# Kernel tuning notes

Hardware: AMD Instinct MI355X
Metric: run time of the kernel (lower is better)

Reference implementation:

```python
import jax, jax.numpy as jnp
import numpy as np

DIM = 512
HEADS = 8
DHEAD = DIM // HEADS
M = DIM // 2          # num_landmarks = 256
ITERS = 6             # pinv iterations
KSIZE = 33            # residual conv kernel (seq axis)
EPS = 1e-5            # LayerNorm eps (torch default)


def moore_penrose_pinv(a, iters=ITERS):
    # a: [b, h, m, m]; iterative Newton-Schulz style pseudo-inverse
    abs_a = jnp.abs(a)
    col = abs_a.sum(-1).max()   # global max of row-sums
    row = abs_a.sum(-2).max()   # global max of col-sums
    z = jnp.swapaxes(a, -1, -2) / (col * row)
    I = jnp.eye(a.shape[-1], dtype=a.dtype)

    def body(z, _):
        az = a @ z
        z = 0.25 * z @ (13.0 * I - az @ (15.0 * I - az @ (7.0 * I - az)))
        return z, None

    z, _ = jax.lax.scan(body, z, None, length=iters)
    return z


def res_conv(v, conv_w):
    # v: [b, h, n, d] treated as NCHW (C=heads), depthwise kernel (33, 1)
    return jax.lax.conv_general_dilated(
        v, conv_w, window_strides=(1, 1),
        padding=((KSIZE // 2, KSIZE // 2), (0, 0)),
        dimension_numbers=('NCHW', 'OIHW', 'NCHW'),
        feature_group_count=HEADS)


def setup_inputs() -> dict:
    key = jax.random.key(0)
    ks = jax.random.split(key, 5)
    b, n = 4, 4096  # n % M == 0 -> no padding branch
    x = jax.random.normal(ks[0], (b, n, DIM), jnp.float32)
    norm_w = jnp.ones((DIM,), jnp.float32)
    norm_b = jnp.zeros((DIM,), jnp.float32)
    Wqkv = jax.random.normal(ks[1], (DIM, 3 * DIM), jnp.float32) * (DIM ** -0.5)
    Wout = jax.random.normal(ks[2], (DIM, DIM), jnp.float32) * (DIM ** -0.5)
    bout = jnp.zeros((DIM,), jnp.float32)
    conv_w = jax.random.normal(ks[3], (HEADS, 1, KSIZE, 1), jnp.float32) * 0.05
    return {"x": x, "norm_w": norm_w, "norm_b": norm_b,
            "Wqkv": Wqkv, "Wout": Wout, "bout": bout, "conv_w": conv_w}


def reference(x, norm_w, norm_b, Wqkv, Wout, bout, conv_w):
    b, n, dim = x.shape
    # LayerNorm
    mu = x.mean(-1, keepdims=True)
    var = ((x - mu) ** 2).mean(-1, keepdims=True)
    xn = (x - mu) * jax.lax.rsqrt(var + EPS) * norm_w + norm_b

    # QKV projection, split heads: [b, h, n, d]
    qkv = xn @ Wqkv
    q, k, v = jnp.split(qkv, 3, axis=-1)
    sh = lambda t: t.reshape(b, n, HEADS, DHEAD).transpose(0, 2, 1, 3)
    q, k, v = sh(q), sh(k), sh(v)
    q = q * (DHEAD ** -0.5)

    # landmarks: mean over consecutive segments of length l = n // M
    l = n // M
    q_l = q.reshape(b, HEADS, M, l, DHEAD).mean(3)  # [b,h,m,d]
    k_l = k.reshape(b, HEADS, M, l, DHEAD).mean(3)

    sim1 = jnp.einsum('bhid,bhjd->bhij', q, k_l)    # [b,h,n,m]
    sim2 = jnp.einsum('bhid,bhjd->bhij', q_l, k_l)  # [b,h,m,m]
    sim3 = jnp.einsum('bhid,bhjd->bhij', q_l, k)    # [b,h,m,n]
    a1 = jax.nn.softmax(sim1, axis=-1)
    a2 = jax.nn.softmax(sim2, axis=-1)
    a3 = jax.nn.softmax(sim3, axis=-1)

    a2_inv = moore_penrose_pinv(a2)
    out = (a1 @ a2_inv) @ (a3 @ v)                  # [b,h,n,d]
    out = out + res_conv(v, conv_w)                  # residual depthwise conv on v

    out = out.transpose(0, 2, 1, 3).reshape(b, n, dim)
    out = out @ Wout + bout                          # to_out (dropout = identity in eval)
    return x + out                                   # TransLayer residual
```

## Files before the change

### kernel.cpp

```cpp
#include <hip/hip_runtime.h>
#include <hip/hip_bf16.h>

#define BB 4
#define NN 4096
#define DIMM 512
#define HH 8
#define DD 64
#define MM 256
#define LL 16
#define BHH 32
#define NROW (BB*NN)
#define KS 33

typedef __attribute__((ext_vector_type(8))) short short8;
typedef __attribute__((ext_vector_type(4))) float float4v;

static __device__ __forceinline__ unsigned short bf16_bits(float v) {
    __hip_bfloat16 h = __float2bfloat16(v);
    return *reinterpret_cast<unsigned short*>(&h);
}

static __device__ __forceinline__ void unpack_bf2(unsigned w, float& lo, float& hi) {
    lo = __uint_as_float(w << 16);
    hi = __uint_as_float(w & 0xffff0000u);
}

static __device__ __forceinline__ void gl_lds16(const void* g, void* l) {
    __builtin_amdgcn_global_load_lds((const __attribute__((address_space(1))) void*)g,
                                     (__attribute__((address_space(3))) void*)l, 16, 0, 0);
}

__launch_bounds__(256)
__global__ void ln_kernel(const float* __restrict__ x,
                          const float* __restrict__ w,
                          const float* __restrict__ bvec,
                          __hip_bfloat16* __restrict__ xn) {
    int row = blockIdx.x;
    int t = threadIdx.x;
    const float* xr = x + (long)row * DIMM;
    float v0 = xr[t];
    float v1 = xr[t + 256];
    __shared__ float red[256];
    red[t] = v0 + v1;
    __syncthreads();
    for (int off = 128; off > 0; off >>= 1) { if (t < off) red[t] += red[t + off]; __syncthreads(); }
    float mu = red[0] * (1.0f / DIMM);
    __syncthreads();
    float d0 = v0 - mu, d1 = v1 - mu;
    red[t] = d0 * d0 + d1 * d1;
    __syncthreads();
    for (int off = 128; off > 0; off >>= 1) { if (t < off) red[t] += red[t + off]; __syncthreads(); }
    float var = red[0] * (1.0f / DIMM);
    float rs = rsqrtf(var + 1e-5f);
    xn[(long)row * DIMM + t]       = __float2bfloat16(d0 * rs * w[t]       + bvec[t]);
    xn[(long)row * DIMM + t + 256] = __float2bfloat16(d1 * rs * w[t + 256] + bvec[t + 256]);
}

__launch_bounds__(256)
__global__ void transpose_bf16(const float* __restrict__ in, __hip_bfloat16* __restrict__ outp,
                               int K, int N) {
    __shared__ float tile[32][33];
    int k0 = blockIdx.y * 32, n0 = blockIdx.x * 32;
    int tx = threadIdx.x & 31, ty = threadIdx.x >> 5;
    #pragma unroll
    for (int i = 0; i < 32; i += 8)
        tile[ty + i][tx] = in[(long)(k0 + ty + i) * N + n0 + tx];
    __syncthreads();
    #pragma unroll
    for (int i = 0; i < 32; i += 8)
        outp[(long)(n0 + ty + i) * K + k0 + tx] = __float2bfloat16(tile[tx][ty + i]);
}

enum { EPI_NONE = 0, EPI_QKV = 1, EPI_OUT = 2 };

template<int EPI>
__launch_bounds__(256)
__global__ void gemm_mfma(const __hip_bfloat16* __restrict__ A,
                          const __hip_bfloat16* __restrict__ Bt,
                          float* __restrict__ C, int M, int N, int K,
                          const float* __restrict__ bias,
                          const float* __restrict__ resid,
                          __hip_bfloat16* __restrict__ qb,
                          __hip_bfloat16* __restrict__ kb,
                          __hip_bfloat16* __restrict__ vtb) {
    __shared__ __hip_bfloat16 As[128][64];
    __shared__ __hip_bfloat16 Bs[128][64];
    const int t = threadIdx.x;
    const int m0 = blockIdx.y * 128, n0 = blockIdx.x * 128;
    const int wave = t >> 6, lane = t & 63;
    const int wrow = wave >> 1, wcol = wave & 1;
    const int lm = lane & 15, quad = lane >> 4;
    const int wbase = wave * 64;

    float4v acc[4][4] = {};

    for (int k0 = 0; k0 < K; k0 += 64) {
        #pragma unroll
        for (int p = 0; p < 4; ++p) {
            int idx = t + p * 256;
            int r = idx >> 3;
            int csrc = ((idx & 7) ^ (r & 7)) * 8;
            int cb = (p * 256 + wbase) * 8;
            gl_lds16(&A[(long)(m0 + r) * K + k0 + csrc], &As[0][0] + cb);
            gl_lds16(&Bt[(long)(n0 + r) * K + k0 + csrc], &Bs[0][0] + cb);
        }
        __syncthreads();
        #pragma unroll
        for (int ks = 0; ks < 64; ks += 32) {
            short8 af[4], bfr[4];
            #pragma unroll
            for (int i = 0; i < 4; ++i) {
                int ra = wrow * 64 + i * 16 + lm;
                int rb = wcol * 64 + i * 16 + lm;
                int g  = (ks >> 3) + quad;
                af[i]  = *(const short8*)&As[ra][(g ^ (ra & 7)) * 8];
                bfr[i] = *(const short8*)&Bs[rb][(g ^ (rb & 7)) * 8];
            }
            #pragma unroll
            for (int i = 0; i < 4; ++i)
                #pragma unroll
                for (int j = 0; j < 4; ++j)
                    acc[i][j] = __builtin_amdgcn_mfma_f32_16x16x32_bf16(af[i], bfr[j], acc[i][j], 0, 0, 0);
        }
        __syncthreads();
    }

    #pragma unroll
    for (int i = 0; i < 4; ++i) {
        #pragma unroll
        for (int j = 0; j < 4; ++j) {
            int rowb = m0 + wrow * 64 + i * 16 + quad * 4;
            int col  = n0 + wcol * 64 + j * 16 + lm;
            if (EPI == EPI_QKV) {
                int b = rowb >> 12, seq = rowb & (NN - 1);
                int which = col >> 9, rem = col & 511;
                int h = rem >> 6, dd = rem & 63;
                int bh = b * HH + h;
                if (which == 0) {
                    #pragma unroll
                    for (int r = 0; r < 4; ++r)
                        qb[((long)bh * NN + seq + r) * DD + dd] = __float2bfloat16(acc[i][j][r] * 0.125f);
                } else if (which == 1) {
                    #pragma unroll
                    for (int r = 0; r < 4; ++r)
                        kb[((long)bh * NN + seq + r) * DD + dd] = __float2bfloat16(acc[i][j][r]);
                } else {
                    union { unsigned long long u; unsigned short s[4]; } pk;
                    #pragma unroll
                    for (int r = 0; r < 4; ++r) pk.s[r] = bf16_bits(acc[i][j][r]);
                    *(unsigned long long*)&vtb[((long)bh * DD + dd) * NN + seq] = pk.u;
                }
            } else {
                #pragma unroll
                for (int r = 0; r < 4; ++r) {
                    int row = rowb + r;
                    C[(long)row * N + col] = acc[i][j][r] + bias[col] + resid[(long)row * N + col];
                }
            }
        }
    }
}

__launch_bounds__(256)
__global__ void gemm_pinv(const __hip_bfloat16* __restrict__ A,
                          const __hip_bfloat16* __restrict__ Bt,
                          __hip_bfloat16* __restrict__ CnBf,
                          float* __restrict__ CnF,
                          __hip_bfloat16* __restrict__ CTbf,
                          float diag, float sgn, float scale) {
    __shared__ __hip_bfloat16 As[64][256];
    __shared__ __hip_bfloat16 Bs[64][256];
    const int t = threadIdx.x;
    const long base = (long)blockIdx.z << 16;
    const int m0 = blockIdx.y * 64, n0 = blockIdx.x * 64;
    const int wave = t >> 6, lane = t & 63;
    const int wr = wave >> 1, wc = wave & 1;
    const int lm = lane & 15, quad = lane >> 4;
    const __hip_bfloat16* Ab = A + base;
    const __hip_bfloat16* Bb = Bt + base;

    #pragma unroll
    for (int p = 0; p < 8; ++p) {
        int idx = t + p * 256;
        int r = idx >> 5;
        int csrc = ((idx & 31) ^ (r & 7)) * 8;
        int cb = idx * 8;
        gl_lds16(&Ab[(long)(m0 + r) * 256 + csrc], &As[0][0] + cb);
        gl_lds16(&Bb[(long)(n0 + r) * 256 + csrc], &Bs[0][0] + cb);
    }
    __syncthreads();

    float4v acc[2][2] = {};
    #pragma unroll
    for (int ks = 0; ks < 256; ks += 32) {
        short8 af[2], bfr[2];
        #pragma unroll
        for (int i = 0; i < 2; ++i) {
            int ra = wr * 32 + i * 16 + lm;
            int rb = wc * 32 + i * 16 + lm;
            int g  = (ks >> 3) + quad;
            af[i]  = *(const short8*)&As[ra][(g ^ (ra & 7)) * 8];
            bfr[i] = *(const short8*)&Bs[rb][(g ^ (rb & 7)) * 8];
        }
        #pragma unroll
        for (int i = 0; i < 2; ++i)
            #pragma unroll
            for (int j = 0; j < 2; ++j)
                acc[i][j] = __builtin_amdgcn_mfma_f32_16x16x32_bf16(af[i], bfr[j], acc[i][j], 0, 0, 0);
    }

    #pragma unroll
    for (int i = 0; i < 2; ++i)
        #pragma unroll
        for (int j = 0; j < 2; ++j) {
            const int rowb = wr * 32 + i * 16 + quad * 4;
            const int col  = wc * 32 + j * 16 + lm;
            union { unsigned long long u; unsigned short s[4]; } pk;
            #pragma unroll
            for (int r = 0; r < 4; ++r) {
                float v = acc[i][j][r] * scale;
                long off = base + (long)(m0 + rowb + r) * 256 + n0 + col;
                if (CnBf) CnBf[off] = __float2bfloat16(v);
                if (CnF)  CnF[off]  = v;
                float tv = sgn * v + ((m0 + rowb + r) == (n0 + col) ? diag : 0.0f);
                pk.s[r] = bf16_bits(tv);
            }
            if (CTbf)
                *(unsigned long long*)&CTbf[base + (long)(n0 + col) * 256 + m0 + rowb] = pk.u;
        }
}

__launch_bounds__(256)
__global__ void pinv_prep(const float* __restrict__ a2, const float* __restrict__ scl,
                          __hip_bfloat16* __restrict__ a2bf, __hip_bfloat16* __restrict__ z0T,
                          __hip_bfloat16* __restrict__ z0n) {
    __shared__ float tl[64][65];
    const int t = threadIdx.x;
    const long base = (long)blockIdx.z << 16;
    const int i0 = blockIdx.y * 64, j0 = blockIdx.x * 64;
    float s = scl[0];
    #pragma unroll
    for (int p = 0; p < 16; ++p) {
        int idx = t + p * 256;
        int r = idx >> 6, c = idx & 63;
        long off = base + (long)(i0 + r) * 256 + j0 + c;
        float v = a2[off];
        a2bf[off] = __float2bfloat16(v);
        float zv = v * s;
        z0T[off] = __float2bfloat16(zv);
        tl[r][c] = zv;
    }
    __syncthreads();
    int r = t & 63;
    #pragma unroll
    for (int u = 0; u < 16; ++u) {
        int c = u * 4 + (t >> 6);
        z0n[base + (long)(j0 + c) * 256 + i0 + r] = __float2bfloat16(tl[r][c]);
    }
}

template<int EPI, bool TRANSB>
__launch_bounds__(256)
__global__ void gemm64(const float* __restrict__ A, const float* __restrict__ Bm,
                       float* __restrict__ C,
                       int M, int N, int K, long sA, long sB, long sC, float alpha) {
    const int bz = blockIdx.z;
    const float* Ab = A + (long)bz * sA;
    const float* Bb = Bm + (long)bz * sB;
    float* Cb = C + (long)bz * sC;

    __shared__ float As[16][64];
    __shared__ float Bs[16][64];

    const int tid = threadIdx.x;
    const int tx = tid & 15;
    const int ty = tid >> 4;
    const int m0 = blockIdx.y * 64;
    const int n0 = blockIdx.x * 64;

    float acc[4][4] = {};

    for (int k0 = 0; k0 < K; k0 += 16) {
        {
            int r  = tid >> 2;
            int kk = (tid & 3) * 4;
            float4 va = *(const float4*)(Ab + (long)(m0 + r) * K + k0 + kk);
            As[kk + 0][r] = va.x; As[kk + 1][r] = va.y; As[kk + 2][r] = va.z; As[kk + 3][r] = va.w;
        }
        if (!TRANSB) {
            int kk = tid >> 4;
            int j  = (tid & 15) * 4;
            float4 vb = *(const float4*)(Bb + (long)(k0 + kk) * N + n0 + j);
            Bs[kk][j + 0] = vb.x; Bs[kk][j + 1] = vb.y; Bs[kk][j + 2] = vb.z; Bs[kk][j + 3] = vb.w;
        } else {
            int j  = tid >> 2;
            int kk = (tid & 3) * 4;
            float4 vb = *(const float4*)(Bb + (long)(n0 + j) * K + k0 + kk);
            Bs[kk + 0][j] = vb.x; Bs[kk + 1][j] = vb.y; Bs[kk + 2][j] = vb.z; Bs[kk + 3][j] = vb.w;
        }
        __syncthreads();
        #pragma unroll
        for (int kk = 0; kk < 16; ++kk) {
            float a0 = As[kk][ty * 4 + 0], a1 = As[kk][ty * 4 + 1];
            float a2 = As[kk][ty * 4 + 2], a3 = As[kk][ty * 4 + 3];
            float b0 = Bs[kk][tx * 4 + 0], b1 = Bs[kk][tx * 4 + 1];
            float b2 = Bs[kk][tx * 4 + 2], b3 = Bs[kk][tx * 4 + 3];
            acc[0][0] += a0 * b0; acc[0][1] += a0 * b1; acc[0][2] += a0 * b2; acc[0][3] += a0 * b3;
            acc[1][0] += a1 * b0; acc[1][1] += a1 * b1; acc[1][2] += a1 * b2; acc[1][3] += a1 * b3;
            acc[2][0] += a2 * b0; acc[2][1] += a2 * b1; acc[2][2] += a2 * b2; acc[2][3] += a2 * b3;
            acc[3][0] += a3 * b0; acc[3][1] += a3 * b1; acc[3][2] += a3 * b2; acc[3][3] += a3 * b3;
        }
        __syncthreads();
    }

    #pragma unroll
    for (int r = 0; r < 4; ++r)
        #pragma unroll
        for (int c = 0; c < 4; ++c)
            Cb[(long)(m0 + ty * 4 + r) * N + n0 + tx * 4 + c] = acc[r][c] * alpha;
}

__global__ void landmark_kernel(const __hip_bfloat16* __restrict__ qb,
                                const __hip_bfloat16* __restrict__ kb,
                                float* __restrict__ q_l, float* __restrict__ k_l,
                                __hip_bfloat16* __restrict__ q_lb,
                                __hip_bfloat16* __restrict__ k_lb) {
    int bh = blockIdx.x >> 8;
    int m  = blockIdx.x & 255;
    int d  = threadIdx.x;
    const __hip_bfloat16* src = (blockIdx.y ? kb : qb) + ((long)bh * NN + m * LL) * DD + d;
    float s = 0.f;
    #pragma unroll
    for (int t = 0; t < LL; ++t) s += __bfloat162float(src[(long)t * DD]);
    s *= (1.0f / LL);
    long off = ((long)bh * MM + m) * DD + d;
    if (blockIdx.y) { k_l[off] = s; k_lb[off] = __float2bfloat16(s); }
    else            { q_l[off] = s; q_lb[off] = __float2bfloat16(s); }
}

__launch_bounds__(256)
__global__ void softmax256_kernel(float* __restrict__ a) {
    long row = blockIdx.x;
    int t = threadIdx.x;
    float* r = a + row * 256;
    float v = r[t];
    __shared__ float red[256];
    red[t] = v;
    __syncthreads();
    for (int off = 128; off > 0; off >>= 1) { if (t < off) red[t] = fmaxf(red[t], red[t + off]); __syncthreads(); }
    float mx = red[0];
    __syncthreads();
    float e = __expf(v - mx);
    red[t] = e;
    __syncthreads();
    for (int off = 128; off > 0; off >>= 1) { if (t < off) red[t] += red[t + off]; __syncthreads(); }
    r[t] = e / red[0];
}

__launch_bounds__(256)
__global__ void redmax_kernel(const float* __restrict__ a2, float* __restrict__ red) {
    int bh = blockIdx.x;
    int t = threadIdx.x;
    const float* Ab = a2 + ((long)bh << 16);
    float cs = 0.f;
    for (int r = 0; r < 256; ++r) cs += Ab[r * 256 + t];
    __shared__ float m2[256];
    m2[t] = cs;
    __syncthreads();
    for (int off = 128; off > 0; off >>= 1) {
        if (t < off) m2[t] = fmaxf(m2[t], m2[t + off]);
        __syncthreads();
    }
    if (t == 0) red[bh] = m2[0];
}

__global__ void scale_kernel(const float* __restrict__ red, float* __restrict__ scl) {
    __shared__ float b[32];
    int t = threadIdx.x;
    b[t] = red[t];
    __syncthreads();
    for (int off = 16; off > 0; off >>= 1) {
        if (t < off) b[t] = fmaxf(b[t], b[t + off]);
        __syncthreads();
    }
    if (t == 0) scl[0] = 1.0f / b[0];
}

__launch_bounds__(256)
__global__ void a3v_mfma(const __hip_bfloat16* __restrict__ qlb,
                         const __hip_bfloat16* __restrict__ kb,
                         const __hip_bfloat16* __restrict__ vtb,
                         float* __restrict__ opart, float* __restrict__ lpart) {
    const int bh = blockIdx.y;
    const int mt = blockIdx.x >> 2;
    const int ns = blockIdx.x & 3;
    const int t = threadIdx.x;
    const int wave = t >> 6, lane = t & 63;
    const int wr = wave >> 1, wc = wave & 1;
    const int lm = lane & 15, quad = lane >> 4;

    __shared__ __hip_bfloat16 Qs[64][72];
    __shared__ __hip_bfloat16 Ks[64][72];
    __shared__ __hip_bfloat16 Vt[64][72];
    __shared__ __hip_bfloat16 Ps[64][72];
    __shared__ float lred[64][32];

    {
        int r = t >> 3, c8 = (t & 7) * 8;
        const __hip_bfloat16* qbase = qlb + ((long)bh * MM + mt * 64) * DD;
        *(uint4*)&Qs[r][c8]      = *(const uint4*)&qbase[(long)r * DD + c8];
        *(uint4*)&Qs[r + 32][c8] = *(const uint4*)&qbase[(long)(r + 32) * DD + c8];
    }

    float4v acc[2][2] = {};
    float lacc[2][4] = {};
    const __hip_bfloat16* kbase = kb + ((long)bh * NN + ns * 1024) * DD;
    const __hip_bfloat16* vbase = vtb + (long)bh * DD * NN + ns * 1024;
    __syncthreads();

    for (int ch = 0; ch < 16; ++ch) {
        {
            int r = t >> 3, c8 = (t & 7) * 8;
            *(uint4*)&Ks[r][c8]      = *(const uint4*)&kbase[(long)(ch * 64 + r) * DD + c8];
            *(uint4*)&Ks[r + 32][c8] = *(const uint4*)&kbase[(long)(ch * 64 + r + 32) * DD + c8];
            *(uint4*)&Vt[r][c8]      = *(const uint4*)&vbase[(long)r * NN + ch * 64 + c8];
            *(uint4*)&Vt[r + 32][c8] = *(const uint4*)&vbase[(long)(r + 32) * NN + ch * 64 + c8];
        }
        __syncthreads();

        float4v s[2][2] = {};
        #pragma unroll
        for (int ks = 0; ks < 64; ks += 32) {
            short8 af[2], bfr[2];
            #pragma unroll
            for (int i = 0; i < 2; ++i) {
                af[i]  = *(const short8*)&Qs[wr * 32 + i * 16 + lm][ks + quad * 8];
                bfr[i] = *(const short8*)&Ks[wc * 32 + i * 16 + lm][ks + quad * 8];
            }
            #pragma unroll
            for (int i = 0; i < 2; ++i)
                #pragma unroll
                for (int j = 0; j < 2; ++j)
                    s[i][j] = __builtin_amdgcn_mfma_f32_16x16x32_bf16(af[i], bfr[j], s[i][j], 0, 0, 0);
        }
        #pragma unroll
        for (int i = 0; i < 2; ++i)
            #pragma unroll
            for (int j = 0; j < 2; ++j)
                #pragma unroll
                for (int r2 = 0; r2 < 4; ++r2) {
                    float e = __expf(s[i][j][r2]);
                    lacc[i][r2] += e;
                    Ps[wr * 32 + i * 16 + quad * 4 + r2][wc * 32 + j * 16 + lm] = __float2bfloat16(e);
                }
        __syncthreads();

        #pragma unroll
        for (int ks = 0; ks < 64; ks += 32) {
            short8 af[2], bfr[2];
            #pragma unroll
            for (int i = 0; i < 2; ++i) {
                af[i]  = *(const short8*)&Ps[wr * 32 + i * 16 + lm][ks + quad * 8];
                bfr[i] = *(const short8*)&Vt[wc * 32 + i * 16 + lm][ks + quad * 8];
            }
            #pragma unroll
            for (int i = 0; i < 2; ++i)
                #pragma unroll
                for (int j = 0; j < 2; ++j)
                    acc[i][j] = __builtin_amdgcn_mfma_f32_16x16x32_bf16(af[i], bfr[j], acc[i][j], 0, 0, 0);
        }
        __syncthreads();
    }

    #pragma unroll
    for (int i = 0; i < 2; ++i)
        #pragma unroll
        for (int r2 = 0; r2 < 4; ++r2)
            lred[wr * 32 + i * 16 + quad * 4 + r2][wc * 16 + lm] = lacc[i][r2];
    __syncthreads();
    if (t < 64) {
        float s = 0.f;
        #pragma unroll
        for (int u = 0; u < 32; ++u) s += lred[t][u];
        lpart[((bh * 4 + mt) * 4 + ns) * 64 + t] = s;
    }
    const long pbase = ((long)((bh * 4 + mt) * 4 + ns)) << 12;
    #pragma unroll
    for (int i = 0; i < 2; ++i)
        #pragma unroll
        for (int j = 0; j < 2; ++j)
            #pragma unroll
            for (int r2 = 0; r2 < 4; ++r2)
                opart[pbase + (long)(wr * 32 + i * 16 + quad * 4 + r2) * 64 + wc * 32 + j * 16 + lm] = acc[i][j][r2];
}

__global__ void a3v_combine(const float* __restrict__ opart, const float* __restrict__ lpart,
                            float* __restrict__ a3v) {
    int idx = blockIdx.x * 256 + threadIdx.x;
    int d  = idx & 63;
    int m  = (idx >> 6) & 255;
    int bh = idx >> 14;
    int mt = m >> 6, r = m & 63;
    int pb = (bh * 4 + mt) * 4;
    float osum = 0.f, lsum = 0.f;
    #pragma unroll
    for (int ns = 0; ns < 4; ++ns) {
        osum += opart[(((long)(pb + ns)) << 12) + r * 64 + d];
        lsum += lpart[(pb + ns) * 64 + r];
    }
    a3v[((long)bh * MM + m) * DD + d] = osum / lsum;
}

__launch_bounds__(256)
__global__ void wmT_kernel(const float* __restrict__ wm, __hip_bfloat16* __restrict__ wtb) {
    __shared__ float tile[64][65];
    const int bh = blockIdx.x;
    const int t = threadIdx.x;
    for (int mc = 0; mc < 4; ++mc) {
        #pragma unroll
        for (int p = 0; p < 16; ++p) {
            int idx = t + p * 256;
            int r = idx >> 6, c = idx & 63;
            tile[r][c] = wm[((long)bh * MM + mc * 64 + r) * DD + c];
        }
        __syncthreads();
        #pragma unroll
        for (int p = 0; p < 16; ++p) {
            int idx = t + p * 256;
            int dd = idx >> 6, m = idx & 63;
            wtb[((long)bh * DD + dd) * MM + mc * 64 + m] = __float2bfloat16(tile[m][dd]);
        }
        __syncthreads();
    }
}

__launch_bounds__(256)
__global__ void attn_out_mfma(const __hip_bfloat16* __restrict__ qb,
                              const __hip_bfloat16* __restrict__ klb,
                              const __hip_bfloat16* __restrict__ wtb,
                              const __hip_bfloat16* __restrict__ vtb,
                              const float* __restrict__ convw,
                              __hip_bfloat16* __restrict__ ctx) {
    const int bh = blockIdx.y;
    const int b = bh >> 3, h = bh & 7;
    const int i0 = blockIdx.x * 64;
    const int t = threadIdx.x;
    const int wave = t >> 6, lane = t & 63;
    const int wr = wave >> 1, wc = wave & 1;
    const int lm = lane & 15, quad = lane >> 4;

    __shared__ __hip_bfloat16 Qs[64][72];
    __shared__ __hip_bfloat16 Ks[64][72];
    __shared__ __hip_bfloat16 Wt[64][72];
    __shared__ __hip_bfloat16 Ps[64][72];
    __shared__ __hip_bfloat16 Vc[64][104];
    __shared__ float lredS[64][2];
    __shared__ float dsum[64];
    __shared__ float cwS[KS];

    if (t < KS) cwS[t] = convw[h * KS + t];

    {
        int r = t >> 3, c8 = (t & 7) * 8;
        const __hip_bfloat16* qbase = qb + ((long)bh * NN + i0) * DD;
        *(uint4*)&Qs[r][c8]      = *(const uint4*)&qbase[(long)r * DD + c8];
        *(uint4*)&Qs[r + 32][c8] = *(const uint4*)&qbase[(long)(r + 32) * DD + c8];
    }
    {
        for (int c = t; c < 768; c += 256) {
            int dd = c / 12, u = c - dd * 12;
            int g0 = i0 - 16 + u * 8;
            const __hip_bfloat16* vrow = vtb + ((long)bh * DD + dd) * NN;
            __align__(16) __hip_bfloat16 tmp[8];
            if (g0 >= 0 && g0 + 8 <= NN) {
                *(uint4*)tmp = *(const uint4*)&vrow[g0];
            } else {
                #pragma unroll
                for (int e = 0; e < 8; ++e) {
                    int g = g0 + e;
                    tmp[e] = (g >= 0 && g < NN) ? vrow[g] : __float2bfloat16(0.f);
                }
            }
            *(uint4*)&Vc[dd][u * 8] = *(uint4*)tmp;
        }
    }

    float4v acc[2][2] = {};
    float lacc[2][4] = {};
    const __hip_bfloat16* klbase = klb + (long)bh * MM * DD;
    const __hip_bfloat16* wbase  = wtb + (long)bh * DD * MM;
    __syncthreads();

    float cwr[KS];
    #pragma unroll
    for (int k = 0; k < KS; ++k) cwr[k] = cwS[k];

    for (int ch = 0; ch < 4; ++ch) {
        {
            int r = t >> 3, c8 = (t & 7) * 8;
            *(uint4*)&Ks[r][c8]      = *(const uint4*)&klbase[(long)(ch * 64 + r) * DD + c8];
            *(uint4*)&Ks[r + 32][c8] = *(const uint4*)&klbase[(long)(ch * 64 + r + 32) * DD + c8];
            *(uint4*)&Wt[r][c8]      = *(const uint4*)&wbase[(long)r * MM + ch * 64 + c8];
            *(uint4*)&Wt[r + 32][c8] = *(const uint4*)&wbase[(long)(r + 32) * MM + ch * 64 + c8];
        }
        __syncthreads();

        float4v s[2][2] = {};
        #pragma unroll
        for (int ks = 0; ks < 64; ks += 32) {
            short8 af[2], bfr[2];
            #pragma unroll
            for (int i = 0; i < 2; ++i) {
                af[i]  = *(const short8*)&Qs[wr * 32 + i * 16 + lm][ks + quad * 8];
                bfr[i] = *(const short8*)&Ks[wc * 32 + i * 16 + lm][ks + quad * 8];
            }
            #pragma unroll
            for (int i = 0; i < 2; ++i)
                #pragma unroll
                for (int j = 0; j < 2; ++j)
                    s[i][j] = __builtin_amdgcn_mfma_f32_16x16x32_bf16(af[i], bfr[j], s[i][j], 0, 0, 0);
        }
        #pragma unroll
        for (int i = 0; i < 2; ++i)
            #pragma unroll
            for (int j = 0; j < 2; ++j)
                #pragma unroll
                for (int r2 = 0; r2 < 4; ++r2) {
                    float e = __expf(s[i][j][r2]);
                    lacc[i][r2] += e;
                    Ps[wr * 32 + i * 16 + quad * 4 + r2][wc * 32 + j * 16 + lm] = __float2bfloat16(e);
                }
        __syncthreads();

        #pragma unroll
        for (int ks = 0; ks < 64; ks += 32) {
            short8 af[2], bfr[2];
            #pragma unroll
            for (int i = 0; i < 2; ++i) {
                af[i]  = *(const short8*)&Ps[wr * 32 + i * 16 + lm][ks + quad * 8];
                bfr[i] = *(const short8*)&Wt[wc * 32 + i * 16 + lm][ks + quad * 8];
            }
            #pragma unroll
            for (int i = 0; i < 2; ++i)
                #pragma unroll
                for (int j = 0; j < 2; ++j)
                    acc[i][j] = __builtin_amdgcn_mfma_f32_16x16x32_bf16(af[i], bfr[j], acc[i][j], 0, 0, 0);
        }
        __syncthreads();
    }

    #pragma unroll
    for (int i = 0; i < 2; ++i)
        #pragma unroll
        for (int r2 = 0; r2 < 4; ++r2) {
            float s = lacc[i][r2];
            s += __shfl_xor(s, 1);
            s += __shfl_xor(s, 2);
            s += __shfl_xor(s, 4);
            s += __shfl_xor(s, 8);
            if (lm == 0) lredS[wr * 32 + i * 16 + quad * 4 + r2][wc] = s;
        }
    __syncthreads();
    if (t < 64) dsum[t] = 1.0f / (lredS[t][0] + lredS[t][1]);
    __syncthreads();

    #pragma unroll
    for (int j = 0; j < 2; ++j) {
        int dd = wc * 32 + j * 16 + lm;
        #pragma unroll
        for (int i = 0; i < 2; ++i) {
            int R = wr * 32 + i * 16 + quad * 4;
            float X[36];
            #pragma unroll
            for (int u = 0; u < 9; ++u) {
                uint2 wv = *(const uint2*)&Vc[dd][R + u * 4];
                unpack_bf2(wv.x, X[u * 4 + 0], X[u * 4 + 1]);
                unpack_bf2(wv.y, X[u * 4 + 2], X[u * 4 + 3]);
            }
            float co[4] = {};
            #pragma unroll
            for (int k = 0; k < KS; ++k) {
                float c = cwr[k];
                co[0] += c * X[k + 0];
                co[1] += c * X[k + 1];
                co[2] += c * X[k + 2];
                co[3] += c * X[k + 3];
            }
            #pragma unroll
            for (int r2 = 0; r2 < 4; ++r2) {
                int row = R + r2;
                ctx[((long)b * NN + i0 + row) * DIMM + h * DD + dd] =
                    __float2bfloat16(acc[i][j][r2] * dsum[row] + co[r2]);
            }
        }
    }
}

extern "C" void kernel_launch(void* const* d_in, const int* in_sizes, int n_in,
                              void* d_out, int out_size, void* d_ws, size_t ws_size,
                              hipStream_t stream) {
    const float* x      = (const float*)d_in[0];
    const float* norm_w = (const float*)d_in[1];
    const float* norm_b = (const float*)d_in[2];
    const float* Wqkv   = (const float*)d_in[3];
    const float* Wout   = (const float*)d_in[4];
    const float* bout   = (const float*)d_in[5];
    const float* conv_w = (const float*)d_in[6];
    float* out = (float*)d_out;

    float* ws = (float*)d_ws;
    size_t o = 0;
    auto alloc = [&](size_t n) { float* p = ws + o; o += n; return p; };
    auto allocb = [&](size_t n) { return (__hip_bfloat16*)alloc((n + 1) / 2); };

    __hip_bfloat16* xn_bf  = allocb((size_t)NROW * DIMM);
    __hip_bfloat16* wqt_bf = allocb((size_t)3 * DIMM * DIMM);
    __hip_bfloat16* wot_bf = allocb((size_t)DIMM * DIMM);
    __hip_bfloat16* ctx_bf = allocb((size_t)NROW * DIMM);
    __hip_bfloat16* q_bf   = allocb((size_t)BHH * NN * DD);
    __hip_bfloat16* k_bf   = allocb((size_t)BHH * NN * DD);
    __hip_bfloat16* vt_bf  = allocb((size_t)BHH * DD * NN);
    __hip_bfloat16* qlb    = allocb((size_t)BHH * MM * DD);
    __hip_bfloat16* klb    = allocb((size_t)BHH * MM * DD);
    __hip_bfloat16* wt_bf  = allocb((size_t)BHH * DD * MM);
    float* q_l  = alloc((size_t)BHH * MM * DD);
    float* k_l  = alloc((size_t)BHH * MM * DD);
    float* a2   = alloc((size_t)BHH * MM * MM);
    float* zb   = alloc((size_t)BHH * MM * MM);
    float* az   = alloc((size_t)BHH * MM * MM);
    float* gb   = alloc((size_t)BHH * MM * MM);
    float* tb   = alloc((size_t)BHH * MM * MM);
    float* z2   = alloc((size_t)BHH * MM * MM);
    float* a3v  = alloc((size_t)BHH * MM * DD);
    float* wm   = alloc((size_t)BHH * MM * DD);
    float* opart = alloc((size_t)BHH * 4 * 4 * 64 * 64);
    float* lpart = alloc((size_t)BHH * 4 * 4 * 64);
    float* red  = alloc(64);
    float* scl  = alloc(64);

    const size_t HB = 1048576;
    __hip_bfloat16* a2bf = (__hip_bfloat16*)az;
    __hip_bfloat16* znA  = (__hip_bfloat16*)(az + HB);
    __hip_bfloat16* znB  = (__hip_bfloat16*)gb;
    __hip_bfloat16* zTA  = (__hip_bfloat16*)(gb + HB);
    __hip_bfloat16* zTB  = (__hip_bfloat16*)tb;
    __hip_bfloat16* azbf = (__hip_bfloat16*)(tb + HB);
    __hip_bfloat16* g1T  = (__hip_bfloat16*)z2;
    __hip_bfloat16* g2T  = (__hip_bfloat16*)(z2 + HB);
    __hip_bfloat16* g3T  = (__hip_bfloat16*)opart;

    ln_kernel<<<NROW, 256, 0, stream>>>(x, norm_w, norm_b, xn_bf);

    transpose_bf16<<<dim3(3 * DIMM / 32, DIMM / 32), 256, 0, stream>>>(Wqkv, wqt_bf, DIMM, 3 * DIMM);
    transpose_bf16<<<dim3(DIMM / 32, DIMM / 32), 256, 0, stream>>>(Wout, wot_bf, DIMM, DIMM);

    gemm_mfma<EPI_QKV><<<dim3(3 * DIMM / 128, NROW / 128), 256, 0, stream>>>(
        xn_bf, wqt_bf, nullptr, NROW, 3 * DIMM, DIMM,
        nullptr, nullptr, q_bf, k_bf, vt_bf);

    landmark_kernel<<<dim3(BHH * MM, 2), 64, 0, stream>>>(q_bf, k_bf, q_l, k_l, qlb, klb);

    gemm64<EPI_NONE, true><<<dim3(4, 4, BHH), 256, 0, stream>>>(
        q_l, k_l, a2, MM, MM, DD, (long)MM * DD, (long)MM * DD, (long)MM * MM, 1.0f);

    softmax256_kernel<<<BHH * MM, 256, 0, stream>>>(a2);

    redmax_kernel<<<BHH, 256, 0, stream>>>(a2, red);
    scale_kernel<<<1, 32, 0, stream>>>(red, scl);

    dim3 g512(4, 4, BHH);
    pinv_prep<<<g512, 256, 0, stream>>>(a2, scl, a2bf, zTA, znA);

    __hip_bfloat16 *zn = znA, *zT = zTA, *zn2 = znB, *zT2 = zTB;
    for (int it = 0; it < 6; ++it) {
        gemm_pinv<<<g512, 256, 0, stream>>>(a2bf, zT, azbf, nullptr, g1T, 7.0f, -1.0f, 1.0f);
        gemm_pinv<<<g512, 256, 0, stream>>>(azbf, g1T, nullptr, nullptr, g2T, 15.0f, -1.0f, 1.0f);
        gemm_pinv<<<g512, 256, 0, stream>>>(azbf, g2T, nullptr, nullptr, g3T, 13.0f, -1.0f, 1.0f);
        gemm_pinv<<<g512, 256, 0, stream>>>(zn, g3T, zn2, (it == 5) ? zb : nullptr, zT2,
                                            0.0f, 1.0f, 0.25f);
        __hip_bfloat16* tmp;
        tmp = zn; zn = zn2; zn2 = tmp;
        tmp = zT; zT = zT2; zT2 = tmp;
    }

    a3v_mfma<<<dim3(16, BHH), 256, 0, stream>>>(qlb, k_bf, vt_bf, opart, lpart);
    a3v_combine<<<BHH * MM * DD / 256, 256, 0, stream>>>(opart, lpart, a3v);

    gemm64<EPI_NONE, false><<<dim3(1, 4, BHH), 256, 0, stream>>>(
        zb, a3v, wm, MM, DD, MM, (long)MM * MM, (long)MM * DD, (long)MM * DD, 1.0f);
    wmT_kernel<<<BHH, 256, 0, stream>>>(wm, wt_bf);

    attn_out_mfma<<<dim3(NN / 64, BHH), 256, 0, stream>>>(
        q_bf, klb, wt_bf, vt_bf, conv_w, ctx_bf);

    gemm_mfma<EPI_OUT><<<dim3(DIMM / 128, NROW / 128), 256, 0, stream>>>(
        ctx_bf, wot_bf, out, NROW, DIMM, DIMM,
        bout, x, nullptr, nullptr, nullptr);
}
```

Measured before the change: 464.6 us.

## Retile pinv GEMM to 128x128 k-looped tiles and run residual conv on MFMA

The pinv GEMM goes from 64x64 output tiles that load the full K=256 into LDS at once to 128x128 tiles that loop over K in 64-wide chunks. This reduces LDS per block and redundant global reads, but cuts the grid from 512 to 128 blocks per launch. Separately, the 33-tap depthwise residual conv in attn_out is recast as a banded Toeplitz matrix in LDS and computed with bf16 MFMAs instead of scalar FMAs. This removes register pressure and FMA work, at the cost of extra LDS and bf16 rounding of the conv weights.

```diff
diff --git a/kernel.cpp b/kernel.cpp
--- a/kernel.cpp
+++ b/kernel.cpp
@@ -18,11 +18,6 @@
 static __device__ __forceinline__ unsigned short bf16_bits(float v) {
     __hip_bfloat16 h = __float2bfloat16(v);
     return *reinterpret_cast<unsigned short*>(&h);
-}
-
-static __device__ __forceinline__ void unpack_bf2(unsigned w, float& lo, float& hi) {
-    lo = __uint_as_float(w << 16);
-    hi = __uint_as_float(w & 0xffff0000u);
 }
 
 static __device__ __forceinline__ void gl_lds16(const void* g, void* l) {
@@ -168,65 +163,69 @@
                           float* __restrict__ CnF,
                           __hip_bfloat16* __restrict__ CTbf,
                           float diag, float sgn, float scale) {
-    __shared__ __hip_bfloat16 As[64][256];
-    __shared__ __hip_bfloat16 Bs[64][256];
+    __shared__ __hip_bfloat16 As[128][64];
+    __shared__ __hip_bfloat16 Bs[128][64];
     const int t = threadIdx.x;
     const long base = (long)blockIdx.z << 16;
-    const int m0 = blockIdx.y * 64, n0 = blockIdx.x * 64;
+    const int m0 = blockIdx.y * 128, n0 = blockIdx.x * 128;
     const int wave = t >> 6, lane = t & 63;
-    const int wr = wave >> 1, wc = wave & 1;
+    const int wrow = wave >> 1, wcol = wave & 1;
     const int lm = lane & 15, quad = lane >> 4;
+    const int wbase = wave * 64;
     const __hip_bfloat16* Ab = A + base;
     const __hip_bfloat16* Bb = Bt + base;
 
-    #pragma unroll
-    for (int p = 0; p < 8; ++p) {
-        int idx = t + p * 256;
-        int r = idx >> 5;
-        int csrc = ((idx & 31) ^ (r & 7)) * 8;
-        int cb = idx * 8;
-        gl_lds16(&Ab[(long)(m0 + r) * 256 + csrc], &As[0][0] + cb);
-        gl_lds16(&Bb[(long)(n0 + r) * 256 + csrc], &Bs[0][0] + cb);
-    }
-    __syncthreads();
-
-    float4v acc[2][2] = {};
-    #pragma unroll
-    for (int ks = 0; ks < 256; ks += 32) {
-        short8 af[2], bfr[2];
-        #pragma unroll
-        for (int i = 0; i < 2; ++i) {
-            int ra = wr * 32 + i * 16 + lm;
-            int rb = wc * 32 + i * 16 + lm;
-            int g  = (ks >> 3) + quad;
-            af[i]  = *(const short8*)&As[ra][(g ^ (ra & 7)) * 8];
-            bfr[i] = *(const short8*)&Bs[rb][(g ^ (rb & 7)) * 8];
-        }
-        #pragma unroll
-        for (int i = 0; i < 2; ++i)
-            #pragma unroll
-            for (int j = 0; j < 2; ++j)
-                acc[i][j] = __builtin_amdgcn_mfma_f32_16x16x32_bf16(af[i], bfr[j], acc[i][j], 0, 0, 0);
-    }
-
-    #pragma unroll
-    for (int i = 0; i < 2; ++i)
-        #pragma unroll
-        for (int j = 0; j < 2; ++j) {
-            const int rowb = wr * 32 + i * 16 + quad * 4;
-            const int col  = wc * 32 + j * 16 + lm;
+    float4v acc[4][4] = {};
+
+    for (int k0 = 0; k0 < 256; k0 += 64) {
+        #pragma unroll
+        for (int p = 0; p < 4; ++p) {
+            int idx = t + p * 256;
+            int r = idx >> 3;
+            int csrc = ((idx & 7) ^ (r & 7)) * 8;
+            int cb = (p * 256 + wbase) * 8;
+            gl_lds16(&Ab[(long)(m0 + r) * 256 + k0 + csrc], &As[0][0] + cb);
+            gl_lds16(&Bb[(long)(n0 + r) * 256 + k0 + csrc], &Bs[0][0] + cb);
+        }
+        __syncthreads();
+        #pragma unroll
+        for (int ks = 0; ks < 64; ks += 32) {
+            short8 af[4], bfr[4];
+            #pragma unroll
+            for (int i = 0; i < 4; ++i) {
+                int ra = wrow * 64 + i * 16 + lm;
+                int rb = wcol * 64 + i * 16 + lm;
+                int g  = (ks >> 3) + quad;
+                af[i]  = *(const short8*)&As[ra][(g ^ (ra & 7)) * 8];
+                bfr[i] = *(const short8*)&Bs[rb][(g ^ (rb & 7)) * 8];
+            }
+            #pragma unroll
+            for (int i = 0; i < 4; ++i)
+                #pragma unroll
+                for (int j = 0; j < 4; ++j)
+                    acc[i][j] = __builtin_amdgcn_mfma_f32_16x16x32_bf16(af[i], bfr[j], acc[i][j], 0, 0, 0);
+        }
+        __syncthreads();
+    }
+
+    #pragma unroll
+    for (int i = 0; i < 4; ++i)
+        #pragma unroll
+        for (int j = 0; j < 4; ++j) {
+            const int rowb = m0 + wrow * 64 + i * 16 + quad * 4;
+            const int col  = n0 + wcol * 64 + j * 16 + lm;
             union { unsigned long long u; unsigned short s[4]; } pk;
             #pragma unroll
             for (int r = 0; r < 4; ++r) {
                 float v = acc[i][j][r] * scale;
-                long off = base + (long)(m0 + rowb + r) * 256 + n0 + col;
+                long off = base + (long)(rowb + r) * 256 + col;
                 if (CnBf) CnBf[off] = __float2bfloat16(v);
                 if (CnF)  CnF[off]  = v;
-                float tv = sgn * v + ((m0 + rowb + r) == (n0 + col) ? diag : 0.0f);
+                float tv = sgn * v + ((rowb + r) == col ? diag : 0.0f);
                 pk.s[r] = bf16_bits(tv);
             }
             if (CTbf)
-                *(unsigned long long*)&CTbf[base + (long)(n0 + col) * 256 + m0 + rowb] = pk.u;
+                *(unsigned long long*)&CTbf[base + (long)col * 256 + rowb] = pk.u;
         }
 }
 
@@ -554,6 +553,7 @@
     __shared__ __hip_bfloat16 Wt[64][72];
     __shared__ __hip_bfloat16 Ps[64][72];
     __shared__ __hip_bfloat16 Vc[64][104];
+    __shared__ __hip_bfloat16 Tpl[64][104];
     __shared__ float lredS[64][2];
     __shared__ float dsum[64];
     __shared__ float cwS[KS];
@@ -591,9 +591,18 @@
     const __hip_bfloat16* wbase  = wtb + (long)bh * DD * MM;
     __syncthreads();
 
-    float cwr[KS];
-    #pragma unroll
-    for (int k = 0; k < KS; ++k) cwr[k] = cwS[k];
+    {
+        int r  = t >> 2;
+        int c0 = (t & 3) * 24;
+        #pragma unroll
+        for (int u = 0; u < 12; ++u) {
+            int c = c0 + u * 2;
+            int d0 = c - r, d1 = c + 1 - r;
+            unsigned short lo = (d0 >= 0 && d0 < KS) ? bf16_bits(cwS[d0]) : (unsigned short)0;
+            unsigned short hi = (d1 >= 0 && d1 < KS) ? bf16_bits(cwS[d1]) : (unsigned short)0;
+            *(unsigned*)&Tpl[r][c] = ((unsigned)hi << 16) | lo;
+        }
+    }
 
     for (int ch = 0; ch < 4; ++ch) {
         {
@@ -649,6 +658,22 @@
         __syncthreads();
     }
 
+    float4v accC[2][2] = {};
+    #pragma unroll
+    for (int ks = 0; ks < 96; ks += 32) {
+        short8 af[2], bfr[2];
+        #pragma unroll
+        for (int i = 0; i < 2; ++i) {
+            af[i]  = *(const short8*)&Tpl[wr * 32 + i * 16 + lm][ks + quad * 8];
+            bfr[i] = *(const short8*)&Vc[wc * 32 + i * 16 + lm][ks + quad * 8];
+        }
+        #pragma unroll
+        for (int i = 0; i < 2; ++i)
+            #pragma unroll
+            for (int j = 0; j < 2; ++j)
+                accC[i][j] = __builtin_amdgcn_mfma_f32_16x16x32_bf16(af[i], bfr[j], accC[i][j], 0, 0, 0);
+    }
+
     #pragma unroll
     for (int i = 0; i < 2; ++i)
         #pragma unroll
@@ -670,27 +695,11 @@
         #pragma unroll
         for (int i = 0; i < 2; ++i) {
             int R = wr * 32 + i * 16 + quad * 4;
-            float X[36];
-            #pragma unroll
-            for (int u = 0; u < 9; ++u) {
-                uint2 wv = *(const uint2*)&Vc[dd][R + u * 4];
-                unpack_bf2(wv.x, X[u * 4 + 0], X[u * 4 + 1]);
-                unpack_bf2(wv.y, X[u * 4 + 2], X[u * 4 + 3]);
-            }
-            float co[4] = {};
-            #pragma unroll
-            for (int k = 0; k < KS; ++k) {
-                float c = cwr[k];
-                co[0] += c * X[k + 0];
-                co[1] += c * X[k + 1];
-                co[2] += c * X[k + 2];
-                co[3] += c * X[k + 3];
-            }
             #pragma unroll
             for (int r2 = 0; r2 < 4; ++r2) {
                 int row = R + r2;
                 ctx[((long)b * NN + i0 + row) * DIMM + h * DD + dd] =
-                    __float2bfloat16(acc[i][j][r2] * dsum[row] + co[r2]);
+                    __float2bfloat16(acc[i][j][r2] * dsum[row] + accC[i][j][r2]);
             }
         }
     }
@@ -768,16 +777,16 @@
     redmax_kernel<<<BHH, 256, 0, stream>>>(a2, red);
     scale_kernel<<<1, 32, 0, stream>>>(red, scl);
 
-    dim3 g512(4, 4, BHH);
-    pinv_prep<<<g512, 256, 0, stream>>>(a2, scl, a2bf, zTA, znA);
-
+    pinv_prep<<<dim3(4, 4, BHH), 256, 0, stream>>>(a2, scl, a2bf, zTA, znA);
+
+    dim3 gp(2, 2, BHH);
     __hip_bfloat16 *zn = znA, *zT = zTA, *zn2 = znB, *zT2 = zTB;
     for (int it = 0; it < 6; ++it) {
-        gemm_pinv<<<g512, 256, 0, stream>>>(a2bf, zT, azbf, nullptr, g1T, 7.0f, -1.0f, 1.0f);
-        gemm_pinv<<<g512, 256, 0, stream>>>(azbf, g1T, nullptr, nullptr, g2T, 15.0f, -1.0f, 1.0f);
-        gemm_pinv<<<g512, 256, 0, stream>>>(azbf, g2T, nullptr, nullptr, g3T, 13.0f, -1.0f, 1.0f);
-        gemm_pinv<<<g512, 256, 0, stream>>>(zn, g3T, zn2, (it == 5) ? zb : nullptr, zT2,
-                                            0.0f, 1.0f, 0.25f);
+        gemm_pinv<<<gp, 256, 0, stream>>>(a2bf, zT, azbf, nullptr, g1T, 7.0f, -1.0f, 1.0f);
+        gemm_pinv<<<gp, 256, 0, stream>>>(azbf, g1T, nullptr, nullptr, g2T, 15.0f, -1.0f, 1.0f);
+        gemm_pinv<<<gp, 256, 0, stream>>>(azbf, g2T, nullptr, nullptr, g3T, 13.0f, -1.0f, 1.0f);
+        gemm_pinv<<<gp, 256, 0, stream>>>(zn, g3T, zn2, (it == 5) ? zb : nullptr, zT2,
+                                          0.0f, 1.0f, 0.25f);
         __hip_bfloat16* tmp;
         tmp = zn; zn = zn2; zn2 = tmp;
         tmp = zT; zT = zT2; zT2 = tmp;
```

Measured after the change: 524.5 us. 12.9% more time.

## Prefetch K/V tiles into registers, MFMA residual conv, parallelize column-sum reduction

Applied to the files above, without the earlier changes.

The a3v and output-attention kernels now load the next K/V (or K/W) chunk into registers while computing the current one, and use a barrier that waits only on LDS traffic instead of a full __syncthreads. The depthwise residual conv is rewritten as a banded Toeplitz matrix built in shared memory and multiplied with MFMA instead of a scalar 33-tap loop. Row-sum reductions use wave shuffles instead of a large shared array. The column-sum max for the pinv scale is split across 8x more blocks with a larger final reduction. The changes trade register pressure and a bf16-rounded conv weight matrix for more overlap and less scalar work.

```diff
diff --git a/kernel.cpp b/kernel.cpp
--- a/kernel.cpp
+++ b/kernel.cpp
@@ -20,14 +20,13 @@
     return *reinterpret_cast<unsigned short*>(&h);
 }
 
-static __device__ __forceinline__ void unpack_bf2(unsigned w, float& lo, float& hi) {
-    lo = __uint_as_float(w << 16);
-    hi = __uint_as_float(w & 0xffff0000u);
-}
-
 static __device__ __forceinline__ void gl_lds16(const void* g, void* l) {
     __builtin_amdgcn_global_load_lds((const __attribute__((address_space(1))) void*)g,
                                      (__attribute__((address_space(3))) void*)l, 16, 0, 0);
+}
+
+static __device__ __forceinline__ void bar_nv() {
+    asm volatile("s_waitcnt lgkmcnt(0)\ns_barrier" ::: "memory");
 }
 
 __launch_bounds__(256)
@@ -359,27 +358,38 @@
 
 __launch_bounds__(256)
 __global__ void redmax_kernel(const float* __restrict__ a2, float* __restrict__ red) {
-    int bh = blockIdx.x;
+    int blk = blockIdx.x;
+    int bh = blk >> 3, cg = blk & 7;
     int t = threadIdx.x;
-    const float* Ab = a2 + ((long)bh << 16);
-    float cs = 0.f;
-    for (int r = 0; r < 256; ++r) cs += Ab[r * 256 + t];
-    __shared__ float m2[256];
-    m2[t] = cs;
-    __syncthreads();
-    for (int off = 128; off > 0; off >>= 1) {
-        if (t < off) m2[t] = fmaxf(m2[t], m2[t + off]);
-        __syncthreads();
-    }
-    if (t == 0) red[bh] = m2[0];
-}
-
+    const float* Ab = a2 + ((long)bh << 16) + cg * 32;
+    int c = t & 31, rg = t >> 5;
+    float s = 0.f;
+    for (int r = rg * 32; r < rg * 32 + 32; ++r) s += Ab[(long)r * 256 + c];
+    __shared__ float m[256];
+    m[t] = s;
+    __syncthreads();
+    if (t < 32) {
+        float cs = 0.f;
+        #pragma unroll
+        for (int g = 0; g < 8; ++g) cs += m[t + 32 * g];
+        m[t] = cs;
+    }
+    __syncthreads();
+    if (t == 0) {
+        float mx = m[0];
+        #pragma unroll
+        for (int i = 1; i < 32; ++i) mx = fmaxf(mx, m[i]);
+        red[blk] = mx;
+    }
+}
+
+__launch_bounds__(256)
 __global__ void scale_kernel(const float* __restrict__ red, float* __restrict__ scl) {
-    __shared__ float b[32];
+    __shared__ float b[256];
     int t = threadIdx.x;
     b[t] = red[t];
     __syncthreads();
-    for (int off = 16; off > 0; off >>= 1) {
+    for (int off = 128; off > 0; off >>= 1) {
         if (t < off) b[t] = fmaxf(b[t], b[t + off]);
         __syncthreads();
     }
@@ -398,35 +408,43 @@
     const int wave = t >> 6, lane = t & 63;
     const int wr = wave >> 1, wc = wave & 1;
     const int lm = lane & 15, quad = lane >> 4;
+    const int r8 = t >> 3, c8 = (t & 7) * 8;
 
     __shared__ __hip_bfloat16 Qs[64][72];
     __shared__ __hip_bfloat16 Ks[64][72];
     __shared__ __hip_bfloat16 Vt[64][72];
     __shared__ __hip_bfloat16 Ps[64][72];
-    __shared__ float lred[64][32];
+    __shared__ float lredS[64][2];
 
     {
-        int r = t >> 3, c8 = (t & 7) * 8;
         const __hip_bfloat16* qbase = qlb + ((long)bh * MM + mt * 64) * DD;
-        *(uint4*)&Qs[r][c8]      = *(const uint4*)&qbase[(long)r * DD + c8];
-        *(uint4*)&Qs[r + 32][c8] = *(const uint4*)&qbase[(long)(r + 32) * DD + c8];
+        *(uint4*)&Qs[r8][c8]      = *(const uint4*)&qbase[(long)r8 * DD + c8];
+        *(uint4*)&Qs[r8 + 32][c8] = *(const uint4*)&qbase[(long)(r8 + 32) * DD + c8];
     }
 
     float4v acc[2][2] = {};
     float lacc[2][4] = {};
     const __hip_bfloat16* kbase = kb + ((long)bh * NN + ns * 1024) * DD;
     const __hip_bfloat16* vbase = vtb + (long)bh * DD * NN + ns * 1024;
-    __syncthreads();
+
+    uint4 kv0 = *(const uint4*)&kbase[(long)r8 * DD + c8];
+    uint4 kv1 = *(const uint4*)&kbase[(long)(r8 + 32) * DD + c8];
+    uint4 vv0 = *(const uint4*)&vbase[(long)r8 * NN + c8];
+    uint4 vv1 = *(const uint4*)&vbase[(long)(r8 + 32) * NN + c8];
+    bar_nv();
 
     for (int ch = 0; ch < 16; ++ch) {
-        {
-            int r = t >> 3, c8 = (t & 7) * 8;
-            *(uint4*)&Ks[r][c8]      = *(const uint4*)&kbase[(long)(ch * 64 + r) * DD + c8];
-            *(uint4*)&Ks[r + 32][c8] = *(const uint4*)&kbase[(long)(ch * 64 + r + 32) * DD + c8];
-            *(uint4*)&Vt[r][c8]      = *(const uint4*)&vbase[(long)r * NN + ch * 64 + c8];
-            *(uint4*)&Vt[r + 32][c8] = *(const uint4*)&vbase[(long)(r + 32) * NN + ch * 64 + c8];
-        }
-        __syncthreads();
+        *(uint4*)&Ks[r8][c8]      = kv0;
+        *(uint4*)&Ks[r8 + 32][c8] = kv1;
+        *(uint4*)&Vt[r8][c8]      = vv0;
+        *(uint4*)&Vt[r8 + 32][c8] = vv1;
+        if (ch < 15) {
+            kv0 = *(const uint4*)&kbase[(long)((ch + 1) * 64 + r8) * DD + c8];
+            kv1 = *(const uint4*)&kbase[(long)((ch + 1) * 64 + r8 + 32) * DD + c8];
+            vv0 = *(const uint4*)&vbase[(long)r8 * NN + (ch + 1) * 64 + c8];
+            vv1 = *(const uint4*)&vbase[(long)(r8 + 32) * NN + (ch + 1) * 64 + c8];
+        }
+        bar_nv();
 
         float4v s[2][2] = {};
         #pragma unroll
@@ -453,7 +471,7 @@
                     lacc[i][r2] += e;
                     Ps[wr * 32 + i * 16 + quad * 4 + r2][wc * 32 + j * 16 + lm] = __float2bfloat16(e);
                 }
-        __syncthreads();
+        bar_nv();
 
         #pragma unroll
         for (int ks = 0; ks < 64; ks += 32) {
@@ -469,21 +487,23 @@
                 for (int j = 0; j < 2; ++j)
                     acc[i][j] = __builtin_amdgcn_mfma_f32_16x16x32_bf16(af[i], bfr[j], acc[i][j], 0, 0, 0);
         }
-        __syncthreads();
+        bar_nv();
     }
 
     #pragma unroll
     for (int i = 0; i < 2; ++i)
         #pragma unroll
-        for (int r2 = 0; r2 < 4; ++r2)
-            lred[wr * 32 + i * 16 + quad * 4 + r2][wc * 16 + lm] = lacc[i][r2];
-    __syncthreads();
-    if (t < 64) {
-        float s = 0.f;
-        #pragma unroll
-        for (int u = 0; u < 32; ++u) s += lred[t][u];
-        lpart[((bh * 4 + mt) * 4 + ns) * 64 + t] = s;
-    }
+        for (int r2 = 0; r2 < 4; ++r2) {
+            float s = lacc[i][r2];
+            s += __shfl_xor(s, 1);
+            s += __shfl_xor(s, 2);
+            s += __shfl_xor(s, 4);
+            s += __shfl_xor(s, 8);
+            if (lm == 0) lredS[wr * 32 + i * 16 + quad * 4 + r2][wc] = s;
+        }
+    __syncthreads();
+    if (t < 64)
+        lpart[((bh * 4 + mt) * 4 + ns) * 64 + t] = lredS[t][0] + lredS[t][1];
     const long pbase = ((long)((bh * 4 + mt) * 4 + ns)) << 12;
     #pragma unroll
     for (int i = 0; i < 2; ++i)
@@ -548,23 +568,23 @@
     const int wave = t >> 6, lane = t & 63;
     const int wr = wave >> 1, wc = wave & 1;
     const int lm = lane & 15, quad = lane >> 4;
+    const int r8 = t >> 3, c8 = (t & 7) * 8;
 
     __shared__ __hip_bfloat16 Qs[64][72];
-    __shared__ __hip_bfloat16 Ks[64][72];
-    __shared__ __hip_bfloat16 Wt[64][72];
+    __shared__ __hip_bfloat16 KW[2][64][72];
     __shared__ __hip_bfloat16 Ps[64][72];
     __shared__ __hip_bfloat16 Vc[64][104];
     __shared__ float lredS[64][2];
     __shared__ float dsum[64];
     __shared__ float cwS[KS];
+    __hip_bfloat16 (*Tpl)[104] = reinterpret_cast<__hip_bfloat16 (*)[104]>(&KW[0][0][0]);
 
     if (t < KS) cwS[t] = convw[h * KS + t];
 
     {
-        int r = t >> 3, c8 = (t & 7) * 8;
         const __hip_bfloat16* qbase = qb + ((long)bh * NN + i0) * DD;
-        *(uint4*)&Qs[r][c8]      = *(const uint4*)&qbase[(long)r * DD + c8];
-        *(uint4*)&Qs[r + 32][c8] = *(const uint4*)&qbase[(long)(r + 32) * DD + c8];
+        *(uint4*)&Qs[r8][c8]      = *(const uint4*)&qbase[(long)r8 * DD + c8];
+        *(uint4*)&Qs[r8 + 32][c8] = *(const uint4*)&qbase[(long)(r8 + 32) * DD + c8];
     }
     {
         for (int c = t; c < 768; c += 256) {
@@ -584,26 +604,61 @@
             *(uint4*)&Vc[dd][u * 8] = *(uint4*)tmp;
         }
     }
+    __syncthreads();
+
+    {
+        int r  = t >> 2;
+        int c0 = (t & 3) * 24;
+        #pragma unroll
+        for (int u = 0; u < 12; ++u) {
+            int c = c0 + u * 2;
+            int d0 = c - r, d1 = c + 1 - r;
+            unsigned short lo = (d0 >= 0 && d0 < KS) ? bf16_bits(cwS[d0]) : (unsigned short)0;
+            unsigned short hi = (d1 >= 0 && d1 < KS) ? bf16_bits(cwS[d1]) : (unsigned short)0;
+            *(unsigned*)&Tpl[r][c] = ((unsigned)hi << 16) | lo;
+        }
+    }
+    bar_nv();
+
+    const __hip_bfloat16* klbase = klb + (long)bh * MM * DD;
+    const __hip_bfloat16* wbase  = wtb + (long)bh * DD * MM;
+    uint4 kv0 = *(const uint4*)&klbase[(long)r8 * DD + c8];
+    uint4 kv1 = *(const uint4*)&klbase[(long)(r8 + 32) * DD + c8];
+    uint4 wv0 = *(const uint4*)&wbase[(long)r8 * MM + c8];
+    uint4 wv1 = *(const uint4*)&wbase[(long)(r8 + 32) * MM + c8];
+
+    float4v accC[2][2] = {};
+    #pragma unroll
+    for (int ks = 0; ks < 96; ks += 32) {
+        short8 af[2], bfr[2];
+        #pragma unroll
+        for (int i = 0; i < 2; ++i) {
+            af[i]  = *(const short8*)&Tpl[wr * 32 + i * 16 + lm][ks + quad * 8];
+            bfr[i] = *(const short8*)&Vc[wc * 32 + i * 16 + lm][ks + quad * 8];
+        }
+        #pragma unroll
+        for (int i = 0; i < 2; ++i)
+            #pragma unroll
+            for (int j = 0; j < 2; ++j)
+                accC[i][j] = __builtin_amdgcn_mfma_f32_16x16x32_bf16(af[i], bfr[j], accC[i][j], 0, 0, 0);
+    }
+    bar_nv();
 
     float4v acc[2][2] = {};
     float lacc[2][4] = {};
-    const __hip_bfloat16* klbase = klb + (long)bh * MM * DD;
-    const __hip_bfloat16* wbase  = wtb + (long)bh * DD * MM;
-    __syncthreads();
-
-    float cwr[KS];
-    #pragma unroll
-    for (int k = 0; k < KS; ++k) cwr[k] = cwS[k];
 
     for (int ch = 0; ch < 4; ++ch) {
-        {
-            int r = t >> 3, c8 = (t & 7) * 8;
-            *(uint4*)&Ks[r][c8]      = *(const uint4*)&klbase[(long)(ch * 64 + r) * DD + c8];
-            *(uint4*)&Ks[r + 32][c8] = *(const uint4*)&klbase[(long)(ch * 64 + r + 32) * DD + c8];
-            *(uint4*)&Wt[r][c8]      = *(const uint4*)&wbase[(long)r * MM + ch * 64 + c8];
-            *(uint4*)&Wt[r + 32][c8] = *(const uint4*)&wbase[(long)(r + 32) * MM + ch * 64 + c8];
-        }
-        __syncthreads();
+        *(uint4*)&KW[0][r8][c8]      = kv0;
+        *(uint4*)&KW[0][r8 + 32][c8] = kv1;
+        *(uint4*)&KW[1][r8][c8]      = wv0;
+        *(uint4*)&KW[1][r8 + 32][c8] = wv1;
+        if (ch < 3) {
+            kv0 = *(const uint4*)&klbase[(long)((ch + 1) * 64 + r8) * DD + c8];
+            kv1 = *(const uint4*)&klbase[(long)((ch + 1) * 64 + r8 + 32) * DD + c8];
+            wv0 = *(const uint4*)&wbase[(long)r8 * MM + (ch + 1) * 64 + c8];
+            wv1 = *(const uint4*)&wbase[(long)(r8 + 32) * MM + (ch + 1) * 64 + c8];
+        }
+        bar_nv();
 
         float4v s[2][2] = {};
         #pragma unroll
@@ -612,7 +667,7 @@
             #pragma unroll
             for (int i = 0; i < 2; ++i) {
                 af[i]  = *(const short8*)&Qs[wr * 32 + i * 16 + lm][ks + quad * 8];
-                bfr[i] = *(const short8*)&Ks[wc * 32 + i * 16 + lm][ks + quad * 8];
+                bfr[i] = *(const short8*)&KW[0][wc * 32 + i * 16 + lm][ks + quad * 8];
             }
             #pragma unroll
             for (int i = 0; i < 2; ++i)
@@ -630,7 +685,7 @@
                     lacc[i][r2] += e;
                     Ps[wr * 32 + i * 16 + quad * 4 + r2][wc * 32 + j * 16 + lm] = __float2bfloat16(e);
                 }
-        __syncthreads();
+        bar_nv();
 
         #pragma unroll
         for (int ks = 0; ks < 64; ks += 32) {
@@ -638,7 +693,7 @@
             #pragma unroll
             for (int i = 0; i < 2; ++i) {
                 af[i]  = *(const short8*)&Ps[wr * 32 + i * 16 + lm][ks + quad * 8];
-                bfr[i] = *(const short8*)&Wt[wc * 32 + i * 16 + lm][ks + quad * 8];
+                bfr[i] = *(const short8*)&KW[1][wc * 32 + i * 16 + lm][ks + quad * 8];
             }
             #pragma unroll
             for (int i = 0; i < 2; ++i)
@@ -646,7 +701,7 @@
                 for (int j = 0; j < 2; ++j)
                     acc[i][j] = __builtin_amdgcn_mfma_f32_16x16x32_bf16(af[i], bfr[j], acc[i][j], 0, 0, 0);
         }
-        __syncthreads();
+        bar_nv();
     }
 
     #pragma unroll
@@ -670,27 +725,11 @@
         #pragma unroll
         for (int i = 0; i < 2; ++i) {
             int R = wr * 32 + i * 16 + quad * 4;
-            float X[36];
-            #pragma unroll
-            for (int u = 0; u < 9; ++u) {
-                uint2 wv = *(const uint2*)&Vc[dd][R + u * 4];
-                unpack_bf2(wv.x, X[u * 4 + 0], X[u * 4 + 1]);
-                unpack_bf2(wv.y, X[u * 4 + 2], X[u * 4 + 3]);
-            }
-            float co[4] = {};
-            #pragma unroll
-            for (int k = 0; k < KS; ++k) {
-                float c = cwr[k];
-                co[0] += c * X[k + 0];
-                co[1] += c * X[k + 1];
-                co[2] += c * X[k + 2];
-                co[3] += c * X[k + 3];
-            }
             #pragma unroll
             for (int r2 = 0; r2 < 4; ++r2) {
                 int row = R + r2;
                 ctx[((long)b * NN + i0 + row) * DIMM + h * DD + dd] =
-                    __float2bfloat16(acc[i][j][r2] * dsum[row] + co[r2]);
+                    __float2bfloat16(acc[i][j][r2] * dsum[row] + accC[i][j][r2]);
             }
         }
     }
@@ -735,7 +774,7 @@
     float* wm   = alloc((size_t)BHH * MM * DD);
     float* opart = alloc((size_t)BHH * 4 * 4 * 64 * 64);
     float* lpart = alloc((size_t)BHH * 4 * 4 * 64);
-    float* red  = alloc(64);
+    float* red  = alloc(256);
     float* scl  = alloc(64);
 
     const size_t HB = 1048576;
@@ -765,8 +804,8 @@
 
     softmax256_kernel<<<BHH * MM, 256, 0, stream>>>(a2);
 
-    redmax_kernel<<<BHH, 256, 0, stream>>>(a2, red);
-    scale_kernel<<<1, 32, 0, stream>>>(red, scl);
+    redmax_kernel<<<BHH * 8, 256, 0, stream>>>(a2, red);
+    scale_kernel<<<1, 256, 0, stream>>>(red, scl);
 
     dim3 g512(4, 4, BHH);
     pinv_prep<<<g512, 256, 0, stream>>>(a2, scl, a2bf, zTA, znA);
```

Result: faster. 451.0 us (-2.9%).
